# Kernel optimization log

Hardware: AMD Instinct MI355X
Metric: run time of the kernel (lower is better)

The kernel has to match this reference:

```python
import jax, jax.numpy as jnp
import numpy as np

B, S, D, H = 2, 2048, 1024, 16
HD = D // H  # 64
ROPE_BASE = 10000.0


def _rope_tables(seq_len, head_dim):
    pos = jnp.arange(seq_len, dtype=jnp.float32)
    inv_freq = 1.0 / (ROPE_BASE ** (jnp.arange(0, head_dim, 2, dtype=jnp.float32) / head_dim))
    ang = pos[:, None] * inv_freq[None, :]            # [S, HD/2]
    emb = jnp.concatenate([ang, ang], axis=-1)        # [S, HD]
    return jnp.cos(emb), jnp.sin(emb)


def setup_inputs() -> dict:
    key = jax.random.key(0)
    k0, k1, k2 = jax.random.split(key, 3)
    x = jax.random.normal(k0, (B, S, D), dtype=jnp.float32)
    Wq = jax.random.normal(k1, (D, D), dtype=jnp.float32) * 0.02
    Wv = jax.random.normal(k2, (D, D), dtype=jnp.float32) * 0.02
    cos, sin = _rope_tables(S, HD)
    return {"x": x, "Wq": Wq, "Wv": Wv, "cos": cos, "sin": sin}


def _rotate_half(u):
    h = u.shape[-1] // 2
    return jnp.concatenate([-u[..., h:], u[..., :h]], axis=-1)


def reference(x, Wq, Wv, cos, sin):
    b, s, d = x.shape
    h, hd = H, d // H
    # NOTE: source module has xk = self.query(x) (key uses query weights) -- preserved.
    xq = (x @ Wq.T).reshape(b, s, h, hd)
    xk = (x @ Wq.T).reshape(b, s, h, hd)
    xv = (x @ Wv.T).reshape(b, s, h, hd)
    c = cos[None, :, None, :]  # [1,S,1,HD]
    sn = sin[None, :, None, :]
    q = xq * c + _rotate_half(xq) * sn
    k = xk * c + _rotate_half(xk) * sn
    q = q.transpose(0, 2, 1, 3)   # [B,H,S,HD]
    k = k.transpose(0, 2, 1, 3)
    v = xv.transpose(0, 2, 1, 3)
    scale = 1.0 / jnp.sqrt(jnp.asarray(hd, dtype=q.dtype))
    scores = jnp.einsum('bhqd,bhkd->bhqk', q, k) * scale  # [B,H,S,S]
    causal = jnp.tril(jnp.ones((s, s), dtype=bool))
    scores = jnp.where(causal[None, None, :, :], scores, jnp.finfo(scores.dtype).min)
    probs = jax.nn.softmax(scores, axis=-1)
    out = jnp.einsum('bhqk,bhkd->bhqd', probs, v)
    return out.transpose(0, 2, 1, 3).reshape(b, s, d)
```

## Files before the change

### kernel.cpp

```cpp
#include <hip/hip_runtime.h>


typedef float f32x4 __attribute__((ext_vector_type(4)));
typedef short s16x8 __attribute__((ext_vector_type(8)));

__device__ inline unsigned short f2bf(float f) {
  union { float f; unsigned u; } v; v.f = f;
  unsigned r = v.u + 0x7FFFu + ((v.u >> 16) & 1u);
  return (unsigned short)(r >> 16);
}

__device__ inline void gload16(const unsigned short* g, unsigned short* l) {
  __builtin_amdgcn_global_load_lds(
      (const __attribute__((address_space(1))) unsigned int*)g,
      (__attribute__((address_space(3))) unsigned int*)l, 16, 0, 0);
}

__global__ __launch_bounds__(256) void convert_all(
    const float* __restrict__ x, const float* __restrict__ wq,
    const float* __restrict__ wv, unsigned short* __restrict__ xb,
    unsigned short* __restrict__ wqb, unsigned short* __restrict__ wvb) {
  int i = blockIdx.x * 256 + threadIdx.x;
  const float* src; unsigned short* dst; int off;
  if (i < 1048576) { src = x; dst = xb; off = i; }
  else if (i < 1310720) { src = wq; dst = wqb; off = i - 1048576; }
  else { src = wv; dst = wvb; off = i - 1310720; }
  float4 v = ((const float4*)src)[off];
  ushort4 o;
  o.x = f2bf(v.x); o.y = f2bf(v.y); o.z = f2bf(v.z); o.w = f2bf(v.w);
  ((ushort4*)dst)[off] = o;
}

__global__ __launch_bounds__(256, 2) void qv_gemm(
    const unsigned short* __restrict__ A, const unsigned short* __restrict__ Wq,
    const unsigned short* __restrict__ Wv, const float* __restrict__ cosT,
    const float* __restrict__ sinT, unsigned short* __restrict__ Kf,
    unsigned short* __restrict__ Vf) {
  __shared__ unsigned short GS[2][2][128][64];
  int tid = threadIdx.x;
  int isq = blockIdx.x < 256;
  int b256 = blockIdx.x & 255;
  int bm = b256 & 31, bn = b256 >> 5;
  int w = tid >> 6, lane = tid & 63, lr = lane & 15, lg = lane >> 4;
  int wm = w >> 1, wn = w & 1;
  int l8 = lane >> 3, l7 = lane & 7;
  f32x4 acc[4][4] = {};

  const unsigned short* Wp = isq ? Wq : Wv;
  const unsigned short* srcbase =
      (w < 2) ? (A + bm * 128 * 1024) : (Wp + bn * 128 * 1024);
  int ab = w >> 1;

  auto stage = [&](int step) {
    int buf = step & 1, kt = step * 64;
#pragma unroll
    for (int i = 0; i < 8; ++i) {
      int rgrp = (w & 1) * 8 + i;
      int u = rgrp * 8 + l8;
      int ch = l7 ^ (u & 7);
      gload16(srcbase + u * 1024 + kt + ch * 8,
              (unsigned short*)&GS[buf][ab][rgrp * 8][0]);
    }
  };

  stage(0);
  for (int step = 0; step < 16; ++step) {
    int buf = step & 1;
    asm volatile("s_waitcnt vmcnt(0)" ::: "memory");
    __syncthreads();
    if (step + 1 < 16) stage(step + 1);
    s16x8 af[4][2], bfr[4][2];
#pragma unroll
    for (int mf = 0; mf < 4; ++mf)
#pragma unroll
      for (int kk = 0; kk < 2; ++kk)
        af[mf][kk] = *(const s16x8*)
            &GS[buf][0][wm * 64 + mf * 16 + lr][((kk * 4 + lg) ^ (lr & 7)) * 8];
#pragma unroll
    for (int nf = 0; nf < 4; ++nf)
#pragma unroll
      for (int kk = 0; kk < 2; ++kk)
        bfr[nf][kk] = *(const s16x8*)
            &GS[buf][1][wn * 64 + nf * 16 + lr][((kk * 4 + lg) ^ (lr & 7)) * 8];
#pragma unroll
    for (int mf = 0; mf < 4; ++mf)
#pragma unroll
      for (int nf = 0; nf < 4; ++nf)
#pragma unroll
        for (int kk = 0; kk < 2; ++kk)
          acc[mf][nf] = __builtin_amdgcn_mfma_f32_16x16x32_bf16(
              af[mf][kk], bfr[nf][kk], acc[mf][nf], 0, 0, 0);
  }

  int mBase = bm * 128 + wm * 64;
  int nBase = bn * 128 + wn * 64;
  if (isq) {
    __syncthreads();
    unsigned short* Lw = &GS[0][0][0][0] + w * (64 * 72);
    int bq = mBase >> 11;
    int sbase = mBase & 2047;
    int kt = sbase >> 6;
    int h = (nBase >> 6);
    int bh = bq * 16 + h;
#pragma unroll
    for (int mf = 0; mf < 4; ++mf)
#pragma unroll
      for (int j = 0; j < 4; ++j) {
        int sp = mf * 16 + 4 * lg + j;
        int s = sbase + sp;
#pragma unroll
        for (int nf = 0; nf < 4; ++nf) {
          int hd = nf * 16 + lr;
          float self = acc[mf][nf][j];
          float part = (nf < 2) ? -acc[mf][nf + 2][j] : acc[mf][nf - 2][j];
          float val = self * cosT[s * 64 + hd] + part * sinT[s * 64 + hd];
          Lw[sp * 72 + hd] = f2bf(val);
        }
      }
    asm volatile("s_waitcnt lgkmcnt(0)" ::: "memory");
    __builtin_amdgcn_sched_barrier(0);
    unsigned short* KfT = Kf + (size_t)(bh * 32 + kt) * 4096;
#pragma unroll
    for (int i = 0; i < 8; ++i) {
      int kk = i & 1, nfk = i >> 1;
      int lg2 = lane >> 4, lr2 = lane & 15;
      int sp = ((nfk >> 1) << 5) | ((lr2 >> 2) << 3) | ((nfk & 1) << 2) |
               (lr2 & 3);
      int c = kk * 4 + lg2;
      s16x8 vch = *(const s16x8*)&Lw[sp * 72 + c * 8];
      *(s16x8*)&KfT[(i * 64 + lane) * 8] = vch;
    }
  } else {
#pragma unroll
    for (int mf = 0; mf < 4; ++mf) {
      int m0 = mBase + mf * 16 + 4 * lg;
      int b = m0 >> 11, s0 = m0 & 2047;
      int kt = s0 >> 6, w0 = s0 & 63;
      int kkv = w0 >> 5, lg2 = (w0 >> 3) & 3, e0 = w0 & 7;
#pragma unroll
      for (int nf = 0; nf < 4; ++nf) {
        int col = nBase + nf * 16 + lr;
        int h = col >> 6;
        int bh = b * 16 + h;
        ushort4 pk;
        pk.x = f2bf(acc[mf][nf][0]); pk.y = f2bf(acc[mf][nf][1]);
        pk.z = f2bf(acc[mf][nf][2]); pk.w = f2bf(acc[mf][nf][3]);
        int idx2 = (((((bh * 32 + kt) * 4 + nf) * 2 + kkv) * 64) +
                    lg2 * 16 + lr) * 8 + e0;
        *(ushort4*)&Vf[idx2] = pk;
      }
    }
  }
}

__global__ __launch_bounds__(256, 2) void attn(
    const unsigned short* __restrict__ Kf,
    const unsigned short* __restrict__ Vf,
    float* __restrict__ out) {
  __shared__ float MB[2][2][4][16][17];
  __shared__ float ML[2][2][2][16];
  const float SC = 0.125f * 1.44269504088896f;
  const float THR = 44.0f;
  int tid = threadIdx.x;
  int fid = blockIdx.x;
  int bh = 4 * (fid & 7) + ((fid >> 3) & 3);
  int pp = fid >> 5;
  int w = tid >> 6, lane = tid & 63, lr = lane & 15, lg = lane >> 4;
  int qh = w >> 1, par = w & 1;

  const unsigned short* KfB = Kf + (size_t)bh * 32 * 4096;
  const unsigned short* VfB = Vf + (size_t)bh * 32 * 4096;
  int b = bh >> 4, h = bh & 15;

  s16x8 kf[4][2], vf[4][2];
  auto loadK = [&](int kt_) {
#pragma unroll
    for (int nf = 0; nf < 4; ++nf)
#pragma unroll
      for (int kk = 0; kk < 2; ++kk)
        kf[nf][kk] = *(const s16x8*)
            &KfB[(((kt_ * 4 + nf) * 2 + kk) * 64 + lane) * 8];
  };
  auto loadV = [&](int kt_) {
#pragma unroll
    for (int nf = 0; nf < 4; ++nf)
#pragma unroll
      for (int kk = 0; kk < 2; ++kk)
        vf[nf][kk] = *(const s16x8*)
            &VfB[(((kt_ * 4 + nf) * 2 + kk) * 64 + lane) * 8];
  };

#pragma unroll 1
  for (int pass = 0; pass < 2; ++pass) {
    int qt = pass ? pp : (31 - pp);
    int q0 = qt * 64;

    s16x8 aq[2][2];
#pragma unroll
    for (int qs = 0; qs < 2; ++qs) {
      int qr = q0 + qh * 32 + 16 * qs + lr;
      int ktq = qr >> 6, w64 = qr & 63;
      int nfq = ((w64 >> 5) << 1) | ((w64 >> 2) & 1);
      int r31 = w64 & 31;
      int lr2 = ((r31 >> 3) << 2) | (r31 & 3);
#pragma unroll
      for (int kk = 0; kk < 2; ++kk)
        aq[qs][kk] = *(const s16x8*)
            &KfB[((((ktq * 4 + nfq) * 2 + kk) * 64) + lg * 16 + lr2) * 8];
    }

    f32x4 o[2][4] = {};
    float m_[2] = {-1e30f, -1e30f}, l_[2] = {0.f, 0.f};

    int kt = par;
    bool active = kt <= qt;
    if (active) { loadK(kt); loadV(kt); }
    while (active) {
      f32x4 sa[2][4];
#pragma unroll
      for (int qs = 0; qs < 2; ++qs)
#pragma unroll
        for (int nf = 0; nf < 4; ++nf) sa[qs][nf] = (f32x4){0.f, 0.f, 0.f, 0.f};
#pragma unroll
      for (int kk = 0; kk < 2; ++kk)
#pragma unroll
        for (int nf = 0; nf < 4; ++nf)
#pragma unroll
          for (int qs = 0; qs < 2; ++qs)
            sa[qs][nf] = __builtin_amdgcn_mfma_f32_16x16x32_bf16(
                kf[nf][kk], aq[qs][kk], sa[qs][nf], 0, 0, 0);

      int ktn = kt + 2;
      bool more = ktn <= qt;
      if (more) loadK(ktn);

      if (kt == qt) {
#pragma unroll
        for (int qs = 0; qs < 2; ++qs) {
          int qglob = q0 + qh * 32 + 16 * qs + lr;
#pragma unroll
          for (int nf = 0; nf < 4; ++nf) {
            int kc = kt * 64 + 8 * lg + 4 * (nf & 1) + 32 * (nf >> 1);
#pragma unroll
            for (int j = 0; j < 4; ++j)
              if (kc + j > qglob) sa[qs][nf][j] = -3e38f;
          }
        }
      }
      float tm[2];
      float worst = -3e38f;
#pragma unroll
      for (int qs = 0; qs < 2; ++qs) {
        float t = sa[qs][0][0];
#pragma unroll
        for (int nf = 0; nf < 4; ++nf)
#pragma unroll
          for (int j = 0; j < 4; ++j) t = fmaxf(t, sa[qs][nf][j]);
        tm[qs] = t;
        worst = fmaxf(worst, t - m_[qs]);
      }
      if (!__all(worst <= THR)) {
#pragma unroll
        for (int qs = 0; qs < 2; ++qs) {
          float rm = fmaxf(tm[qs], __shfl_xor(tm[qs], 16));
          rm = fmaxf(rm, __shfl_xor(rm, 32));
          float mn = fmaxf(m_[qs], rm);
          float alpha = exp2f((m_[qs] - mn) * SC);
          m_[qs] = mn; l_[qs] *= alpha;
#pragma unroll
          for (int j = 0; j < 4; ++j) {
            float aj = __shfl(alpha, 4 * lg + j);
#pragma unroll
            for (int nf = 0; nf < 4; ++nf) o[qs][nf][j] *= aj;
          }
        }
      }
      unsigned cpk[2][8];
#pragma unroll
      for (int qs = 0; qs < 2; ++qs) {
        float msc = m_[qs] * SC;
#pragma unroll
        for (int nf = 0; nf < 4; ++nf) {
          float p0 = exp2f(fmaf(sa[qs][nf][0], SC, -msc));
          float p1 = exp2f(fmaf(sa[qs][nf][1], SC, -msc));
          float p2 = exp2f(fmaf(sa[qs][nf][2], SC, -msc));
          float p3 = exp2f(fmaf(sa[qs][nf][3], SC, -msc));
          l_[qs] += (p0 + p1) + (p2 + p3);
          unsigned r0, r1;
          asm("v_cvt_pk_bf16_f32 %0, %1, %2" : "=v"(r0) : "v"(p0), "v"(p1));
          asm("v_cvt_pk_bf16_f32 %0, %1, %2" : "=v"(r1) : "v"(p2), "v"(p3));
          cpk[qs][nf * 2] = r0; cpk[qs][nf * 2 + 1] = r1;
        }
      }
      s16x8 pav[2][2];
#pragma unroll
      for (int qs = 0; qs < 2; ++qs)
#pragma unroll
        for (int kk = 0; kk < 2; ++kk) {
          union { unsigned u[4]; s16x8 v; } pa;
          pa.u[0] = cpk[qs][4 * kk + 0]; pa.u[1] = cpk[qs][4 * kk + 1];
          pa.u[2] = cpk[qs][4 * kk + 2]; pa.u[3] = cpk[qs][4 * kk + 3];
          pav[qs][kk] = pa.v;
        }
#pragma unroll
      for (int kk = 0; kk < 2; ++kk)
#pragma unroll
        for (int nf = 0; nf < 4; ++nf)
#pragma unroll
          for (int qs = 0; qs < 2; ++qs)
            o[qs][nf] = __builtin_amdgcn_mfma_f32_16x16x32_bf16(
                pav[qs][kk], vf[nf][kk], o[qs][nf], 0, 0, 0);
      if (more) loadV(ktn);
      kt = ktn; active = more;
    }

#pragma unroll
    for (int qs = 0; qs < 2; ++qs) {
      float t = l_[qs];
      t += __shfl_xor(t, 16); t += __shfl_xor(t, 32);
      l_[qs] = t;
    }
    if (par) {
#pragma unroll
      for (int qs = 0; qs < 2; ++qs) {
#pragma unroll
        for (int nf = 0; nf < 4; ++nf)
#pragma unroll
          for (int j = 0; j < 4; ++j)
            MB[qh][qs][nf][4 * lg + j][lr] = o[qs][nf][j];
        if (lg == 0) {
          ML[qh][qs][0][lr] = m_[qs];
          ML[qh][qs][1][lr] = l_[qs];
        }
      }
    }
    __syncthreads();
    if (!par) {
#pragma unroll
      for (int qs = 0; qs < 2; ++qs) {
        float m1 = ML[qh][qs][0][lr];
        float l1 = ML[qh][qs][1][lr];
        float ms = fmaxf(m_[qs], m1);
        float a0 = exp2f((m_[qs] - ms) * SC), a1 = exp2f((m1 - ms) * SC);
        float inv = 1.0f / (a0 * l_[qs] + a1 * l1);
#pragma unroll
        for (int j = 0; j < 4; ++j) {
          float c0 = __shfl(a0 * inv, 4 * lg + j);
          float c1 = __shfl(a1 * inv, 4 * lg + j);
#pragma unroll
          for (int nf = 0; nf < 4; ++nf) {
            float o1 = MB[qh][qs][nf][4 * lg + j][lr];
            int q = q0 + qh * 32 + 16 * qs + 4 * lg + j;
            out[(b * 2048 + q) * 1024 + h * 64 + nf * 16 + lr] =
                c0 * o[qs][nf][j] + c1 * o1;
          }
        }
      }
    }
    __syncthreads();
  }
}

extern "C" void kernel_launch(void* const* d_in, const int* in_sizes, int n_in,
                              void* d_out, int out_size, void* d_ws, size_t ws_size,
                              hipStream_t stream) {
  const float* x = (const float*)d_in[0];
  const float* Wq = (const float*)d_in[1];
  const float* Wv = (const float*)d_in[2];
  const float* cosT = (const float*)d_in[3];
  const float* sinT = (const float*)d_in[4];
  float* out = (float*)d_out;

  unsigned short* xb = (unsigned short*)d_ws;
  unsigned short* wqb = xb + 4 * 1024 * 1024;
  unsigned short* wvb = wqb + 1024 * 1024;
  unsigned short* Kfb = wvb + 1024 * 1024;
  unsigned short* Vfb = Kfb + 4 * 1024 * 1024;

  convert_all<<<6144, 256, 0, stream>>>(x, Wq, Wv, xb, wqb, wvb);
  qv_gemm<<<512, 256, 0, stream>>>(xb, wqb, wvb, cosT, sinT, Kfb, Vfb);
  attn<<<512, 256, 0, stream>>>(Kfb, Vfb, out);
}
```

Before: 68.37 us.

## Split attention KV range four ways per 32-row query tile

Each attention block now handles 32 query rows instead of 64, and all four waves split the key tiles of that strip (stride 4) instead of two waves per 32-row half. Partial outputs from three waves are merged through shared memory with a four-way log-sum-exp combine. The grid doubles to 1024 blocks and launch bounds allow four blocks per CU, aiming for better load balance and occupancy on the causal workload. In exchange there is more combine overhead, and the last key tile is partly masked for 32-row strips.

```diff
diff --git a/kernel.cpp b/kernel.cpp
--- a/kernel.cpp
+++ b/kernel.cpp
@@ -153,21 +153,19 @@
   }
 }
 
-__global__ __launch_bounds__(256, 2) void attn(
+__global__ __launch_bounds__(256, 4) void attn(
     const unsigned short* __restrict__ Kf,
     const unsigned short* __restrict__ Vf,
     float* __restrict__ out) {
-  __shared__ float MB[2][2][4][16][17];
-  __shared__ float ML[2][2][2][16];
+  __shared__ float MB[3][2][4][16][17];
+  __shared__ float ML[3][2][2][16];
   const float SC = 0.125f * 1.44269504088896f;
   const float THR = 44.0f;
   int tid = threadIdx.x;
   int fid = blockIdx.x;
   int bh = 4 * (fid & 7) + ((fid >> 3) & 3);
-  int pp = fid >> 5;
-  int w = tid >> 6, lane = tid & 63, lr = lane & 15, lg = lane >> 4;
-  int qh = w >> 1, par = w & 1;
-
+  int p = fid >> 5;
+  int par = tid >> 6, lane = tid & 63, lr = lane & 15, lg = lane >> 4;
   const unsigned short* KfB = Kf + (size_t)bh * 32 * 4096;
   const unsigned short* VfB = Vf + (size_t)bh * 32 * 4096;
   int b = bh >> 4, h = bh & 15;
@@ -192,13 +190,14 @@
 
 #pragma unroll 1
   for (int pass = 0; pass < 2; ++pass) {
-    int qt = pass ? pp : (31 - pp);
-    int q0 = qt * 64;
+    int s = pass ? p : (63 - p);
+    int q0 = s * 32;
+    int ktmax = s >> 1;
 
     s16x8 aq[2][2];
 #pragma unroll
     for (int qs = 0; qs < 2; ++qs) {
-      int qr = q0 + qh * 32 + 16 * qs + lr;
+      int qr = q0 + 16 * qs + lr;
       int ktq = qr >> 6, w64 = qr & 63;
       int nfq = ((w64 >> 5) << 1) | ((w64 >> 2) & 1);
       int r31 = w64 & 31;
@@ -213,7 +212,7 @@
     float m_[2] = {-1e30f, -1e30f}, l_[2] = {0.f, 0.f};
 
     int kt = par;
-    bool active = kt <= qt;
+    bool active = kt <= ktmax;
     if (active) { loadK(kt); loadV(kt); }
     while (active) {
       f32x4 sa[2][4];
@@ -230,14 +229,14 @@
             sa[qs][nf] = __builtin_amdgcn_mfma_f32_16x16x32_bf16(
                 kf[nf][kk], aq[qs][kk], sa[qs][nf], 0, 0, 0);
 
-      int ktn = kt + 2;
-      bool more = ktn <= qt;
+      int ktn = kt + 4;
+      bool more = ktn <= ktmax;
       if (more) loadK(ktn);
 
-      if (kt == qt) {
+      if (kt == ktmax) {
 #pragma unroll
         for (int qs = 0; qs < 2; ++qs) {
-          int qglob = q0 + qh * 32 + 16 * qs + lr;
+          int qglob = q0 + 16 * qs + lr;
 #pragma unroll
           for (int nf = 0; nf < 4; ++nf) {
             int kc = kt * 64 + 8 * lg + 4 * (nf & 1) + 32 * (nf >> 1);
@@ -327,32 +326,37 @@
         for (int nf = 0; nf < 4; ++nf)
 #pragma unroll
           for (int j = 0; j < 4; ++j)
-            MB[qh][qs][nf][4 * lg + j][lr] = o[qs][nf][j];
+            MB[par - 1][qs][nf][4 * lg + j][lr] = o[qs][nf][j];
         if (lg == 0) {
-          ML[qh][qs][0][lr] = m_[qs];
-          ML[qh][qs][1][lr] = l_[qs];
+          ML[par - 1][qs][0][lr] = m_[qs];
+          ML[par - 1][qs][1][lr] = l_[qs];
         }
       }
     }
     __syncthreads();
-    if (!par) {
+    if (par == 0) {
 #pragma unroll
       for (int qs = 0; qs < 2; ++qs) {
-        float m1 = ML[qh][qs][0][lr];
-        float l1 = ML[qh][qs][1][lr];
-        float ms = fmaxf(m_[qs], m1);
+        float m1 = ML[0][qs][0][lr], l1 = ML[0][qs][1][lr];
+        float m2 = ML[1][qs][0][lr], l2 = ML[1][qs][1][lr];
+        float m3 = ML[2][qs][0][lr], l3 = ML[2][qs][1][lr];
+        float ms = fmaxf(fmaxf(m_[qs], m1), fmaxf(m2, m3));
         float a0 = exp2f((m_[qs] - ms) * SC), a1 = exp2f((m1 - ms) * SC);
-        float inv = 1.0f / (a0 * l_[qs] + a1 * l1);
+        float a2 = exp2f((m2 - ms) * SC), a3 = exp2f((m3 - ms) * SC);
+        float inv = 1.0f / (a0 * l_[qs] + a1 * l1 + a2 * l2 + a3 * l3);
 #pragma unroll
         for (int j = 0; j < 4; ++j) {
           float c0 = __shfl(a0 * inv, 4 * lg + j);
           float c1 = __shfl(a1 * inv, 4 * lg + j);
+          float c2 = __shfl(a2 * inv, 4 * lg + j);
+          float c3 = __shfl(a3 * inv, 4 * lg + j);
 #pragma unroll
           for (int nf = 0; nf < 4; ++nf) {
-            float o1 = MB[qh][qs][nf][4 * lg + j][lr];
-            int q = q0 + qh * 32 + 16 * qs + 4 * lg + j;
-            out[(b * 2048 + q) * 1024 + h * 64 + nf * 16 + lr] =
-                c0 * o[qs][nf][j] + c1 * o1;
+            int r = 4 * lg + j;
+            float ov = c0 * o[qs][nf][j] + c1 * MB[0][qs][nf][r][lr] +
+                       c2 * MB[1][qs][nf][r][lr] + c3 * MB[2][qs][nf][r][lr];
+            int q = q0 + 16 * qs + r;
+            out[(b * 2048 + q) * 1024 + h * 64 + nf * 16 + lr] = ov;
           }
         }
       }
@@ -379,5 +383,5 @@
 
   convert_all<<<6144, 256, 0, stream>>>(x, Wq, Wv, xb, wqb, wvb);
   qv_gemm<<<512, 256, 0, stream>>>(xb, wqb, wvb, cosT, sinT, Kfb, Vfb);
-  attn<<<512, 256, 0, stream>>>(Kfb, Vfb, out);
-}
+  attn<<<1024, 256, 0, stream>>>(Kfb, Vfb, out);
+}
```

Result: slower. 184.4 us (+169.7%).
